# Kernel tuning notes

Measured on AMD Instinct MI355X. Metric: run time of the kernel, lower is better.

## Reference

```python
import jax, jax.numpy as jnp
import numpy as np


def _lstm_layer(x, w_ih, w_hh, b):
    """Single LSTM layer, PyTorch gate order (i, f, g, o).
    x: [B, T, Din]; w_ih: [4H, Din]; w_hh: [4H, H]; b: [4H] (= b_ih + b_hh).
    Returns hidden states [B, T, H]."""
    H = w_hh.shape[1]
    # Precompute input contribution for all timesteps at once (big GEMM).
    gates_x = jnp.einsum('btd,gd->btg', x, w_ih) + b  # [B, T, 4H]
    gates_t = jnp.swapaxes(gates_x, 0, 1)             # [T, B, 4H]
    B = x.shape[0]
    h0 = jnp.zeros((B, H), x.dtype)
    c0 = jnp.zeros((B, H), x.dtype)

    def step(carry, gx):
        h, c = carry
        g = gx + h @ w_hh.T                           # [B, 4H]
        i, f, gg, o = jnp.split(g, 4, axis=-1)
        i = jax.nn.sigmoid(i)
        f = jax.nn.sigmoid(f)
        gg = jnp.tanh(gg)
        o = jax.nn.sigmoid(o)
        c = f * c + i * gg
        h = o * jnp.tanh(c)
        return (h, c), h

    _, hs = jax.lax.scan(step, (h0, c0), gates_t)     # hs: [T, B, H]
    return jnp.swapaxes(hs, 0, 1)                     # [B, T, H]


def setup_inputs() -> dict:
    key = jax.random.key(0)
    ks = jax.random.split(key, 10)
    B, T, Din = 256, 256, 128
    Hemb = 512   # hidden_size (embed output)
    H = 512      # lstm_hidden_size
    L = 3        # nlayers
    Dout = 1     # output_size

    def unif(k, shape, bound):
        return jax.random.uniform(k, shape, jnp.float32, -bound, bound)

    s_emb = 1.0 / np.sqrt(Din)
    s_lstm = 1.0 / np.sqrt(H)
    s_dec = 1.0 / np.sqrt(H)

    return {
        'x': jax.random.normal(ks[0], (B, T, Din), jnp.float32),
        'embed_W': unif(ks[1], (Hemb, Din), s_emb),
        'embed_b': unif(ks[2], (Hemb,), s_emb),
        # stacked per-layer LSTM weights (hidden_size == lstm_hidden_size)
        'w_ih': unif(ks[3], (L, 4 * H, Hemb), s_lstm),
        'w_hh': unif(ks[4], (L, 4 * H, H), s_lstm),
        'b_ih': unif(ks[5], (L, 4 * H), s_lstm),
        'b_hh': unif(ks[6], (L, 4 * H), s_lstm),
        'dec_W': unif(ks[7], (Dout, H), s_dec),
        'dec_b': unif(ks[8], (Dout,), s_dec),
    }


def reference(x, embed_W, embed_b, w_ih, w_hh, b_ih, b_hh, dec_W, dec_b):
    # embed: Linear(input_size -> hidden_size)
    h = x @ embed_W.T + embed_b                       # [B, T, Hemb]
    # multi-layer LSTM (batch_first), zero initial state
    L = w_ih.shape[0]
    for l in range(L):
        h = _lstm_layer(h, w_ih[l], w_hh[l], b_ih[l] + b_hh[l])
    # decoder on last timestep, then flatten
    out = h[:, -1] @ dec_W.T + dec_b                  # [B, Dout]
    return out.reshape(-1)
```

## Files before the change

kernel.cpp:

```cpp
#include <hip/hip_runtime.h>
#include <hip/hip_fp16.h>
#include <cstdint>


#define TT   256
#define NBAT 256
#define DIN  128
#define HID  512
#define RD   16

typedef _Float16 half_t;
typedef __attribute__((ext_vector_type(8))) _Float16 half8;
typedef __attribute__((ext_vector_type(4))) _Float16 half4v;
typedef __attribute__((ext_vector_type(4))) float f32x4;

__device__ __forceinline__ float sigmoidf_(float x) {
    return 1.f / (1.f + __expf(-x));
}
__device__ __forceinline__ float tanhf_(float x) {
    float xc = fminf(fmaxf(x, -15.f), 15.f);
    float e = __expf(2.f * xc);
    return (e - 1.f) / (e + 1.f);
}

__device__ __forceinline__ half8 ld_cg16(const half_t* p) {
    union { unsigned long long u[2]; half8 v; } r;
    r.u[0] = __hip_atomic_load((const unsigned long long*)p,
                               __ATOMIC_RELAXED, __HIP_MEMORY_SCOPE_AGENT);
    r.u[1] = __hip_atomic_load((const unsigned long long*)p + 1,
                               __ATOMIC_RELAXED, __HIP_MEMORY_SCOPE_AGENT);
    return r.v;
}
__device__ __forceinline__ void st_cg2(half_t* p, float v) {
    half_t h = (half_t)v;
    unsigned short b = __builtin_bit_cast(unsigned short, h);
    __hip_atomic_store((unsigned short*)p, b,
                       __ATOMIC_RELAXED, __HIP_MEMORY_SCOPE_AGENT);
}

__device__ __forceinline__ void phase_out(float* Pl, const f32x4* accn,
                                          int wv, int lane) {
    #pragma unroll
    for (int n = 0; n < 4; ++n)
        #pragma unroll
        for (int q = 0; q < 4; ++q) {
            int prow = (wv << 4) + ((lane >> 4) << 2) + q;
            int cidx = (n << 4) + (lane & 15);
            Pl[prow * 64 + (cidx ^ ((((prow >> 2) ^ prow) & 1) << 4))] = accn[n][q];
        }
}
__device__ __forceinline__ float red_gates(const float* Pl, const float* b4,
                                           int rr, int jj, float& c) {
    float gs[4];
    #pragma unroll
    for (int gt = 0; gt < 4; ++gt) {
        float s = b4[gt];
        int cidx = (gt << 4) + jj;
        #pragma unroll
        for (int w2 = 0; w2 < 4; ++w2) {
            int r0 = (w2 << 4) + rr;
            s += Pl[r0 * 64 + (cidx ^ ((((r0 >> 2) ^ r0) & 1) << 4))];
        }
        gs[gt] = s;
    }
    float ig = sigmoidf_(gs[0]), fg = sigmoidf_(gs[1]);
    float gg = tanhf_(gs[2]), og = sigmoidf_(gs[3]);
    c = fg * c + ig * gg;
    return og * tanhf_(c);
}

__global__ __launch_bounds__(256) void k_w16(const float* __restrict__ wih,
                                             const float* __restrict__ whh,
                                             half_t* __restrict__ wbuf) {
    half8* wb = (half8*)wbuf;
    const int bid = blockIdx.x;
    const int l = bid >> 7;
    const int rem = bid & 127;
    const int hb = rem >> 2, q = rem & 3;
    const int tid = threadIdx.x;
    #pragma unroll
    for (int i = 0; i < 8; ++i) {
        int unit = tid + (i << 8);
        int kit = unit >> 8, n = (unit >> 6) & 3, lane = unit & 63;
        int grow = l * 2048 + n * 512 + hb * 16 + (lane & 15);
        int col = q * 256 + kit * 32 + ((lane >> 4) << 3);
        const float* src = (col < 512) ? (wih + (size_t)grow * HID + col)
                                       : (whh + (size_t)grow * HID + (col - 512));
        float4 u0 = *(const float4*)src;
        float4 u1 = *(const float4*)(src + 4);
        wb[((size_t)(l * 32 + hb) * 4 + q) * 2048 + unit] =
            (half8){(half_t)u0.x, (half_t)u0.y, (half_t)u0.z, (half_t)u0.w,
                    (half_t)u1.x, (half_t)u1.y, (half_t)u1.z, (half_t)u1.w};
    }
}

__global__ __launch_bounds__(256) void k_embed(const float* __restrict__ x,
                                               const float* __restrict__ W,
                                               const float* __restrict__ bias,
                                               half_t* __restrict__ out) {
    extern __shared__ char smem[];
    half_t* Xs = (half_t*)smem;
    half_t* Ws = (half_t*)(smem + 16384);
    const int tid = threadIdx.x;
    const int bk = blockIdx.x;
    const int t = bk >> 2, b0 = (bk & 3) << 6;

    #pragma unroll
    for (int it = 0; it < 8; ++it) {
        int idx = tid + (it << 8);
        int r = idx >> 5, k = (idx & 31) << 2;
        float4 v = *(const float4*)(x + ((size_t)(b0 + r) * TT + t) * DIN + k);
        half4v hv = {(half_t)v.x, (half_t)v.y, (half_t)v.z, (half_t)v.w};
        int byte = r * 256 + ((k * 2) ^ ((r & 7) << 4));
        *(half4v*)((char*)Xs + byte) = hv;
    }
    #pragma unroll 4
    for (int it = 0; it < 64; ++it) {
        int idx = tid + (it << 8);
        int r = idx >> 5, k = (idx & 31) << 2;
        float4 v = *(const float4*)(W + (size_t)r * DIN + k);
        half4v hv = {(half_t)v.x, (half_t)v.y, (half_t)v.z, (half_t)v.w};
        int byte = r * 256 + ((k * 2) ^ ((r & 7) << 4));
        *(half4v*)((char*)Ws + byte) = hv;
    }
    __syncthreads();

    const int lane = tid & 63, wv = tid >> 6;
    f32x4 acc[4][8];
    #pragma unroll
    for (int m = 0; m < 4; ++m)
        #pragma unroll
        for (int n = 0; n < 8; ++n) acc[m][n] = (f32x4){0.f, 0.f, 0.f, 0.f};

    #pragma unroll
    for (int kit = 0; kit < 4; ++kit) {
        int kk = (kit << 5) + ((lane >> 4) << 3);
        half8 a[4];
        #pragma unroll
        for (int m = 0; m < 4; ++m) {
            int r = (m << 4) + (lane & 15);
            int byte = r * 256 + ((kk * 2) ^ ((r & 7) << 4));
            a[m] = *(half8*)((char*)Xs + byte);
        }
        #pragma unroll
        for (int n = 0; n < 8; ++n) {
            int r = (wv << 7) + (n << 4) + (lane & 15);
            int byte = r * 256 + ((kk * 2) ^ ((r & 7) << 4));
            half8 b = *(half8*)((char*)Ws + byte);
            #pragma unroll
            for (int m = 0; m < 4; ++m)
                acc[m][n] = __builtin_amdgcn_mfma_f32_16x16x32_f16(a[m], b, acc[m][n], 0, 0, 0);
        }
    }
    __syncthreads();
    half_t* Os = (half_t*)smem;
    #pragma unroll
    for (int n = 0; n < 8; ++n) {
        int j = (wv << 7) + (n << 4) + (lane & 15);
        float bj = bias[j];
        #pragma unroll
        for (int m = 0; m < 4; ++m)
            #pragma unroll
            for (int r = 0; r < 4; ++r) {
                int mr = (m << 4) + ((lane >> 4) << 2) + r;
                Os[mr * 512 + j] = (half_t)(acc[m][n][r] + bj);
            }
    }
    __syncthreads();
    #pragma unroll
    for (int it = 0; it < 16; ++it) {
        int idx = tid + (it << 8);
        int r = idx >> 6, c = (idx & 63) << 3;
        half8 v = *(half8*)(Os + r * 512 + c);
        *(half8*)(out + ((size_t)t * NBAT + (b0 + r)) * HID + c) = v;
    }
}

__global__ __launch_bounds__(256, 1) void k_rec(const half_t* __restrict__ wbuf,
                                                const half_t* __restrict__ bufE,
                                                half_t* __restrict__ ring0,
                                                half_t* __restrict__ ring1,
                                                half_t* __restrict__ ring2,
                                                half_t* __restrict__ outbuf,
                                                const float* __restrict__ b_ih,
                                                const float* __restrict__ b_hh,
                                                int* __restrict__ flags) {
    extern __shared__ char smem[];
    half8* W2s = (half8*)smem;
    float* Pl = (float*)(smem + 131072);

    const half8* wb = (const half8*)wbuf;
    const int tid = threadIdx.x;
    const int lane = tid & 63, wv = tid >> 6;
    const int g = blockIdx.x & 7;
    const int hb = blockIdx.x >> 3;
    const int b0 = g << 5;
    const int j0 = hb << 4;
    const int rr = tid >> 4;
    const int jj = tid & 15;
    const bool low = (wv < 2);
    const int qw = wv ^ 2;
    const int koff = ((wv & 1) << 8) + ((lane >> 4) << 3);
    bool dead = false;

    half8 Bf0[8][4], Bf1[8][4];
    {
        const half8* w0 = wb + ((size_t)hb * 4 + wv) * 2048;
        const half8* w1 = wb + ((size_t)(32 + hb) * 4 + qw) * 2048;
        #pragma unroll
        for (int kit = 0; kit < 8; ++kit)
            #pragma unroll
            for (int n = 0; n < 4; ++n) {
                Bf0[kit][n] = w0[kit * 256 + n * 64 + lane];
                Bf1[kit][n] = w1[kit * 256 + n * 64 + lane];
            }
    }
    {
        const half8* w2 = wb + (size_t)(64 + hb) * 4 * 2048;
        #pragma unroll 4
        for (int it = 0; it < 32; ++it) {
            int idx = tid + (it << 8);
            W2s[idx] = w2[idx];
        }
    }
    float bias[3][4];
    #pragma unroll
    for (int l = 0; l < 3; ++l)
        #pragma unroll
        for (int gt = 0; gt < 4; ++gt)
            bias[l][gt] = b_ih[(size_t)l * 2048 + gt * HID + j0 + jj] +
                          b_hh[(size_t)l * 2048 + gt * HID + j0 + jj];
    float cA0 = 0.f, cA1 = 0.f, cB0 = 0.f, cB1 = 0.f, cC0 = 0.f, cC1 = 0.f;
    __syncthreads();

    const size_t RNG = (size_t)NBAT * HID;

    for (int r = 0; r < TT + 2; ++r) {
        const bool act0 = (r < TT);
        const bool act1 = (r >= 1 && r <= TT);
        const bool act2 = (r >= 2);

        if (tid < 96 && !dead) {
            int l = tid >> 5;
            int need = r - l; if (need > TT) need = TT;
            if (need > 0) {
                const int* fp = flags + l * 256 + (g << 5) + (tid & 31);
                int guard = 0;
                while (__hip_atomic_load(fp, __ATOMIC_RELAXED,
                                         __HIP_MEMORY_SCOPE_AGENT) < need) {
                    __builtin_amdgcn_s_sleep(1);
                    if (++guard > (1 << 17)) { dead = true; break; }
                }
            }
        }
        __syncthreads();

        half8 p0a[8], p0b[8];
        const size_t rowb = (size_t)(b0 + (lane & 15)) * HID + koff;
        if (low) {
            if (act0) {
                const half_t* ar = bufE + (size_t)r * RNG + rowb;
                #pragma unroll
                for (int kit = 0; kit < 8; ++kit) {
                    p0a[kit] = *(const half8*)(ar + (kit << 5));
                    p0b[kit] = *(const half8*)(ar + (size_t)16 * HID + (kit << 5));
                }
            }
        } else if (act1) {
            const half_t* ar = ring0 + (size_t)((r - 1) & (RD - 1)) * RNG + rowb;
            #pragma unroll
            for (int kit = 0; kit < 8; ++kit) {
                p0a[kit] = ld_cg16(ar + (kit << 5));
                p0b[kit] = ld_cg16(ar + (size_t)16 * HID + (kit << 5));
            }
        }

        f32x4 acc[2][4];

        #pragma unroll
        for (int m = 0; m < 2; ++m)
            #pragma unroll
            for (int n = 0; n < 4; ++n) acc[m][n] = (f32x4){0.f, 0.f, 0.f, 0.f};
        if (act0 && (low || r >= 1)) {
            #pragma unroll
            for (int kit = 0; kit < 8; ++kit)
                #pragma unroll
                for (int n = 0; n < 4; ++n) {
                    acc[0][n] = __builtin_amdgcn_mfma_f32_16x16x32_f16(p0a[kit], Bf0[kit][n], acc[0][n], 0, 0, 0);
                    acc[1][n] = __builtin_amdgcn_mfma_f32_16x16x32_f16(p0b[kit], Bf0[kit][n], acc[1][n], 0, 0, 0);
                }
        }
        half8 p1a[8], p1b[8];
        if (low && r >= 2) {
            const half_t* ar = ring1 + (size_t)((r - 2) & (RD - 1)) * RNG + rowb;
            #pragma unroll
            for (int kit = 0; kit < 8; ++kit) {
                p1a[kit] = ld_cg16(ar + (kit << 5));
                p1b[kit] = ld_cg16(ar + (size_t)16 * HID + (kit << 5));
            }
        }
        {
            half_t* dst = ring0 + (size_t)(r & (RD - 1)) * RNG;
            __syncthreads();
            phase_out(Pl, acc[0], wv, lane);
            __syncthreads();
            if (act0) st_cg2(dst + (size_t)(b0 + rr) * HID + j0 + jj,
                             red_gates(Pl, bias[0], rr, jj, cA0));
            __syncthreads();
            phase_out(Pl, acc[1], wv, lane);
            __syncthreads();
            if (act0) st_cg2(dst + (size_t)(b0 + 16 + rr) * HID + j0 + jj,
                             red_gates(Pl, bias[0], rr, jj, cA1));
        }

        #pragma unroll
        for (int m = 0; m < 2; ++m)
            #pragma unroll
            for (int n = 0; n < 4; ++n) acc[m][n] = (f32x4){0.f, 0.f, 0.f, 0.f};
        if (act1) {
            if (!low) {
                #pragma unroll
                for (int kit = 0; kit < 8; ++kit)
                    #pragma unroll
                    for (int n = 0; n < 4; ++n) {
                        acc[0][n] = __builtin_amdgcn_mfma_f32_16x16x32_f16(p0a[kit], Bf1[kit][n], acc[0][n], 0, 0, 0);
                        acc[1][n] = __builtin_amdgcn_mfma_f32_16x16x32_f16(p0b[kit], Bf1[kit][n], acc[1][n], 0, 0, 0);
                    }
            } else if (r >= 2) {
                #pragma unroll
                for (int kit = 0; kit < 8; ++kit)
                    #pragma unroll
                    for (int n = 0; n < 4; ++n) {
                        acc[0][n] = __builtin_amdgcn_mfma_f32_16x16x32_f16(p1a[kit], Bf1[kit][n], acc[0][n], 0, 0, 0);
                        acc[1][n] = __builtin_amdgcn_mfma_f32_16x16x32_f16(p1b[kit], Bf1[kit][n], acc[1][n], 0, 0, 0);
                    }
            }
        }
        if (!low && r >= 3) {
            const half_t* ar = ring2 + (size_t)((r - 3) & (RD - 1)) * RNG + rowb;
            #pragma unroll
            for (int kit = 0; kit < 8; ++kit) {
                p1a[kit] = ld_cg16(ar + (kit << 5));
                p1b[kit] = ld_cg16(ar + (size_t)16 * HID + (kit << 5));
            }
        }
        {
            half_t* dst = ring1 + (size_t)((r - 1) & (RD - 1)) * RNG;
            __syncthreads();
            phase_out(Pl, acc[0], wv, lane);
            __syncthreads();
            if (act1) st_cg2(dst + (size_t)(b0 + rr) * HID + j0 + jj,
                             red_gates(Pl, bias[1], rr, jj, cB0));
            __syncthreads();
            phase_out(Pl, acc[1], wv, lane);
            __syncthreads();
            if (act1) st_cg2(dst + (size_t)(b0 + 16 + rr) * HID + j0 + jj,
                             red_gates(Pl, bias[1], rr, jj, cB1));
        }

        #pragma unroll
        for (int m = 0; m < 2; ++m)
            #pragma unroll
            for (int n = 0; n < 4; ++n) acc[m][n] = (f32x4){0.f, 0.f, 0.f, 0.f};
        if (act2 && (low || r >= 3)) {
            const half8* w2l = W2s + ((size_t)wv << 11);
            #pragma unroll
            for (int kit = 0; kit < 8; ++kit) {
                half8 B0 = w2l[kit * 256 + 0 * 64 + lane];
                half8 B1 = w2l[kit * 256 + 1 * 64 + lane];
                half8 B2 = w2l[kit * 256 + 2 * 64 + lane];
                half8 B3 = w2l[kit * 256 + 3 * 64 + lane];
                acc[0][0] = __builtin_amdgcn_mfma_f32_16x16x32_f16(p1a[kit], B0, acc[0][0], 0, 0, 0);
                acc[1][0] = __builtin_amdgcn_mfma_f32_16x16x32_f16(p1b[kit], B0, acc[1][0], 0, 0, 0);
                acc[0][1] = __builtin_amdgcn_mfma_f32_16x16x32_f16(p1a[kit], B1, acc[0][1], 0, 0, 0);
                acc[1][1] = __builtin_amdgcn_mfma_f32_16x16x32_f16(p1b[kit], B1, acc[1][1], 0, 0, 0);
                acc[0][2] = __builtin_amdgcn_mfma_f32_16x16x32_f16(p1a[kit], B2, acc[0][2], 0, 0, 0);
                acc[1][2] = __builtin_amdgcn_mfma_f32_16x16x32_f16(p1b[kit], B2, acc[1][2], 0, 0, 0);
                acc[0][3] = __builtin_amdgcn_mfma_f32_16x16x32_f16(p1a[kit], B3, acc[0][3], 0, 0, 0);
                acc[1][3] = __builtin_amdgcn_mfma_f32_16x16x32_f16(p1b[kit], B3, acc[1][3], 0, 0, 0);
            }
        }
        {
            const int t2 = r - 2;
            half_t* dst = ring2 + (size_t)(t2 & (RD - 1)) * RNG;
            __syncthreads();
            phase_out(Pl, acc[0], wv, lane);
            __syncthreads();
            if (act2) {
                float h = red_gates(Pl, bias[2], rr, jj, cC0);
                st_cg2(dst + (size_t)(b0 + rr) * HID + j0 + jj, h);
                if (t2 == TT - 1)
                    st_cg2(outbuf + (size_t)(b0 + rr) * HID + j0 + jj, h);
            }
            __syncthreads();
            phase_out(Pl, acc[1], wv, lane);
            __syncthreads();
            if (act2) {
                float h = red_gates(Pl, bias[2], rr, jj, cC1);
                st_cg2(dst + (size_t)(b0 + 16 + rr) * HID + j0 + jj, h);
                if (t2 == TT - 1)
                    st_cg2(outbuf + (size_t)(b0 + 16 + rr) * HID + j0 + jj, h);
            }
        }

        asm volatile("s_waitcnt vmcnt(0)" ::: "memory");
        __builtin_amdgcn_sched_barrier(0);
        __syncthreads();
        if (tid == 0 && act0)
            __hip_atomic_store(flags + 0 * 256 + (g << 5) + hb, r + 1,
                               __ATOMIC_RELAXED, __HIP_MEMORY_SCOPE_AGENT);
        if (tid == 1 && act1)
            __hip_atomic_store(flags + 1 * 256 + (g << 5) + hb, r,
                               __ATOMIC_RELAXED, __HIP_MEMORY_SCOPE_AGENT);
        if (tid == 2 && act2)
            __hip_atomic_store(flags + 2 * 256 + (g << 5) + hb, r - 1,
                               __ATOMIC_RELAXED, __HIP_MEMORY_SCOPE_AGENT);
    }
}

__global__ __launch_bounds__(256) void k_dec(const half_t* __restrict__ act,
                                             const float* __restrict__ dW,
                                             const float* __restrict__ db,
                                             float* __restrict__ out) {
    int tid = threadIdx.x;
    int bl = tid >> 3, part = tid & 7;
    int b = (blockIdx.x << 5) + bl;
    const half_t* row = act + (size_t)b * HID + (part << 6);
    float s = 0.f;
    #pragma unroll
    for (int i = 0; i < 8; ++i) {
        half8 v = ld_cg16(row + (i << 3));
        const float* wp = dW + (part << 6) + (i << 3);
        #pragma unroll
        for (int u = 0; u < 8; ++u) s += (float)v[u] * wp[u];
    }
    #pragma unroll
    for (int off = 1; off < 8; off <<= 1) s += __shfl_xor(s, off, 64);
    if (part == 0) out[b] = s + db[0];
}

extern "C" void kernel_launch(void* const* d_in, const int* in_sizes, int n_in,
                              void* d_out, int out_size, void* d_ws, size_t ws_size,
                              hipStream_t stream) {
    const float* x = (const float*)d_in[0];
    const float* eW = (const float*)d_in[1];
    const float* eb = (const float*)d_in[2];
    const float* wih = (const float*)d_in[3];
    const float* whh = (const float*)d_in[4];
    const float* bih = (const float*)d_in[5];
    const float* bhh = (const float*)d_in[6];
    const float* dW = (const float*)d_in[7];
    const float* db = (const float*)d_in[8];
    float* out = (float*)d_out;

    const size_t MB = 1u << 20;
    const size_t BUFE_OFF = 0;
    const size_t RING0_OFF = 64 * MB;
    const size_t RING1_OFF = 68 * MB;
    const size_t RING2_OFF = 72 * MB;
    const size_t OUT_OFF = 76 * MB;
    const size_t WBUF_OFF = 80 * MB;
    const size_t FLAG_OFF = 96 * MB;
    if (ws_size < 96 * MB + 65536) return;

    char* ws = (char*)d_ws;
    half_t* bufE = (half_t*)(ws + BUFE_OFF);
    half_t* ring0 = (half_t*)(ws + RING0_OFF);
    half_t* ring1 = (half_t*)(ws + RING1_OFF);
    half_t* ring2 = (half_t*)(ws + RING2_OFF);
    half_t* outbuf = (half_t*)(ws + OUT_OFF);
    half_t* wbuf = (half_t*)(ws + WBUF_OFF);
    int* flags = (int*)(ws + FLAG_OFF);

    hipMemsetAsync(flags, 0, 1024 * sizeof(int), stream);

    (void)hipFuncSetAttribute((const void*)k_embed,
                              hipFuncAttributeMaxDynamicSharedMemorySize, 147456);
    (void)hipFuncSetAttribute((const void*)k_rec,
                              hipFuncAttributeMaxDynamicSharedMemorySize, 147456);

    k_w16<<<384, 256, 0, stream>>>(wih, whh, wbuf);
    k_embed<<<1024, 256, 147456, stream>>>(x, eW, eb, bufE);

    void* args[] = { (void*)&wbuf, (void*)&bufE, (void*)&ring0, (void*)&ring1,
                     (void*)&ring2, (void*)&outbuf, (void*)&bih, (void*)&bhh,
                     (void*)&flags };
    hipError_t ce = hipLaunchCooperativeKernel((const void*)k_rec, dim3(256), dim3(256),
                                               args, 147456, stream);
    if (ce != hipSuccess) {
        k_rec<<<256, 256, 147456, stream>>>(wbuf, bufE, ring0, ring1, ring2,
                                            outbuf, bih, bhh, flags);
    }

    k_dec<<<8, 256, 0, stream>>>(outbuf, dW, db, out);
}
```

Before: 2.970 ms.

## Split recurrent LSTM kernel K-reduction across eight waves per block

Doubles the recurrent kernel's block size to 512 threads so each wave covers a quarter of the hidden dimension, halving per-wave MFMA chains and register-held weight fragments. Partial gate sums from 8 waves are reduced through a larger LDS staging area, with only the first 256 threads applying the gate nonlinearities. Some redundant barriers are removed. The intent is to shorten the per-timestep critical path and improve latency hiding, at the cost of more LDS traffic in the reduction and tighter register limits from the new launch bounds.

Measured after the change: 4.181 ms. +40.8%, slower.

```diff
diff --git a/kernel.cpp b/kernel.cpp
--- a/kernel.cpp
+++ b/kernel.cpp
@@ -39,12 +39,12 @@
 }
 
 __device__ __forceinline__ void phase_out(float* Pl, const f32x4* accn,
-                                          int wv, int lane) {
+                                          int w, int lane) {
     #pragma unroll
     for (int n = 0; n < 4; ++n)
         #pragma unroll
         for (int q = 0; q < 4; ++q) {
-            int prow = (wv << 4) + ((lane >> 4) << 2) + q;
+            int prow = (w << 4) + ((lane >> 4) << 2) + q;
             int cidx = (n << 4) + (lane & 15);
             Pl[prow * 64 + (cidx ^ ((((prow >> 2) ^ prow) & 1) << 4))] = accn[n][q];
         }
@@ -57,8 +57,8 @@
         float s = b4[gt];
         int cidx = (gt << 4) + jj;
         #pragma unroll
-        for (int w2 = 0; w2 < 4; ++w2) {
-            int r0 = (w2 << 4) + rr;
+        for (int w8 = 0; w8 < 8; ++w8) {
+            int r0 = (w8 << 4) + rr;
             s += Pl[r0 * 64 + (cidx ^ ((((r0 >> 2) ^ r0) & 1) << 4))];
         }
         gs[gt] = s;
@@ -176,7 +176,7 @@
     }
 }
 
-__global__ __launch_bounds__(256, 1) void k_rec(const half_t* __restrict__ wbuf,
+__global__ __launch_bounds__(512, 2) void k_rec(const half_t* __restrict__ wbuf,
                                                 const half_t* __restrict__ bufE,
                                                 half_t* __restrict__ ring0,
                                                 half_t* __restrict__ ring1,
@@ -191,24 +191,25 @@
 
     const half8* wb = (const half8*)wbuf;
     const int tid = threadIdx.x;
-    const int lane = tid & 63, wv = tid >> 6;
+    const int lane = tid & 63, w = tid >> 6;
     const int g = blockIdx.x & 7;
     const int hb = blockIdx.x >> 3;
     const int b0 = g << 5;
     const int j0 = hb << 4;
     const int rr = tid >> 4;
     const int jj = tid & 15;
-    const bool low = (wv < 2);
-    const int qw = wv ^ 2;
-    const int koff = ((wv & 1) << 8) + ((lane >> 4) << 3);
+    const bool low = (w < 4);
+    const int wsub = w & 3;
+    const int koff = (wsub << 7) + ((lane >> 4) << 3);
+    const int wq1 = w ^ 4;
     bool dead = false;
 
-    half8 Bf0[8][4], Bf1[8][4];
+    half8 Bf0[4][4], Bf1[4][4];
     {
-        const half8* w0 = wb + ((size_t)hb * 4 + wv) * 2048;
-        const half8* w1 = wb + ((size_t)(32 + hb) * 4 + qw) * 2048;
-        #pragma unroll
-        for (int kit = 0; kit < 8; ++kit)
+        const half8* w0 = wb + ((size_t)hb * 4 + (w >> 1)) * 2048 + ((w & 1) << 10);
+        const half8* w1 = wb + ((size_t)(32 + hb) * 4 + (wq1 >> 1)) * 2048 + ((wq1 & 1) << 10);
+        #pragma unroll
+        for (int kit = 0; kit < 4; ++kit)
             #pragma unroll
             for (int n = 0; n < 4; ++n) {
                 Bf0[kit][n] = w0[kit * 256 + n * 64 + lane];
@@ -218,8 +219,8 @@
     {
         const half8* w2 = wb + (size_t)(64 + hb) * 4 * 2048;
         #pragma unroll 4
-        for (int it = 0; it < 32; ++it) {
-            int idx = tid + (it << 8);
+        for (int it = 0; it < 16; ++it) {
+            int idx = tid + (it << 9);
             W2s[idx] = w2[idx];
         }
     }
@@ -234,6 +235,7 @@
     __syncthreads();
 
     const size_t RNG = (size_t)NBAT * HID;
+    const bool red = (tid < 256);
 
     for (int r = 0; r < TT + 2; ++r) {
         const bool act0 = (r < TT);
@@ -255,13 +257,13 @@
         }
         __syncthreads();
 
-        half8 p0a[8], p0b[8];
+        half8 p0a[4], p0b[4];
         const size_t rowb = (size_t)(b0 + (lane & 15)) * HID + koff;
         if (low) {
             if (act0) {
                 const half_t* ar = bufE + (size_t)r * RNG + rowb;
                 #pragma unroll
-                for (int kit = 0; kit < 8; ++kit) {
+                for (int kit = 0; kit < 4; ++kit) {
                     p0a[kit] = *(const half8*)(ar + (kit << 5));
                     p0b[kit] = *(const half8*)(ar + (size_t)16 * HID + (kit << 5));
                 }
@@ -269,7 +271,7 @@
         } else if (act1) {
             const half_t* ar = ring0 + (size_t)((r - 1) & (RD - 1)) * RNG + rowb;
             #pragma unroll
-            for (int kit = 0; kit < 8; ++kit) {
+            for (int kit = 0; kit < 4; ++kit) {
                 p0a[kit] = ld_cg16(ar + (kit << 5));
                 p0b[kit] = ld_cg16(ar + (size_t)16 * HID + (kit << 5));
             }
@@ -283,35 +285,35 @@
             for (int n = 0; n < 4; ++n) acc[m][n] = (f32x4){0.f, 0.f, 0.f, 0.f};
         if (act0 && (low || r >= 1)) {
             #pragma unroll
-            for (int kit = 0; kit < 8; ++kit)
+            for (int kit = 0; kit < 4; ++kit)
                 #pragma unroll
                 for (int n = 0; n < 4; ++n) {
                     acc[0][n] = __builtin_amdgcn_mfma_f32_16x16x32_f16(p0a[kit], Bf0[kit][n], acc[0][n], 0, 0, 0);
                     acc[1][n] = __builtin_amdgcn_mfma_f32_16x16x32_f16(p0b[kit], Bf0[kit][n], acc[1][n], 0, 0, 0);
                 }
         }
-        half8 p1a[8], p1b[8];
+        half8 p1a[4], p1b[4];
         if (low && r >= 2) {
             const half_t* ar = ring1 + (size_t)((r - 2) & (RD - 1)) * RNG + rowb;
             #pragma unroll
-            for (int kit = 0; kit < 8; ++kit) {
+            for (int kit = 0; kit < 4; ++kit) {
                 p1a[kit] = ld_cg16(ar + (kit << 5));
                 p1b[kit] = ld_cg16(ar + (size_t)16 * HID + (kit << 5));
             }
         }
         {
             half_t* dst = ring0 + (size_t)(r & (RD - 1)) * RNG;
-            __syncthreads();
-            phase_out(Pl, acc[0], wv, lane);
-            __syncthreads();
-            if (act0) st_cg2(dst + (size_t)(b0 + rr) * HID + j0 + jj,
-                             red_gates(Pl, bias[0], rr, jj, cA0));
-            __syncthreads();
-            phase_out(Pl, acc[1], wv, lane);
-            __syncthreads();
-            if (act0) st_cg2(dst + (size_t)(b0 + 16 + rr) * HID + j0 + jj,
-                             red_gates(Pl, bias[0], rr, jj, cA1));
-        }
+            phase_out(Pl, acc[0], w, lane);
+            __syncthreads();
+            if (red && act0) st_cg2(dst + (size_t)(b0 + rr) * HID + j0 + jj,
+                                    red_gates(Pl, bias[0], rr, jj, cA0));
+            __syncthreads();
+            phase_out(Pl, acc[1], w, lane);
+            __syncthreads();
+            if (red && act0) st_cg2(dst + (size_t)(b0 + 16 + rr) * HID + j0 + jj,
+                                    red_gates(Pl, bias[0], rr, jj, cA1));
+        }
+        __syncthreads();
 
         #pragma unroll
         for (int m = 0; m < 2; ++m)
@@ -320,7 +322,7 @@
         if (act1) {
             if (!low) {
                 #pragma unroll
-                for (int kit = 0; kit < 8; ++kit)
+                for (int kit = 0; kit < 4; ++kit)
                     #pragma unroll
                     for (int n = 0; n < 4; ++n) {
                         acc[0][n] = __builtin_amdgcn_mfma_f32_16x16x32_f16(p0a[kit], Bf1[kit][n], acc[0][n], 0, 0, 0);
@@ -328,7 +330,7 @@
                     }
             } else if (r >= 2) {
                 #pragma unroll
-                for (int kit = 0; kit < 8; ++kit)
+                for (int kit = 0; kit < 4; ++kit)
                     #pragma unroll
                     for (int n = 0; n < 4; ++n) {
                         acc[0][n] = __builtin_amdgcn_mfma_f32_16x16x32_f16(p1a[kit], Bf1[kit][n], acc[0][n], 0, 0, 0);
@@ -339,33 +341,33 @@
         if (!low && r >= 3) {
             const half_t* ar = ring2 + (size_t)((r - 3) & (RD - 1)) * RNG + rowb;
             #pragma unroll
-            for (int kit = 0; kit < 8; ++kit) {
+            for (int kit = 0; kit < 4; ++kit) {
                 p1a[kit] = ld_cg16(ar + (kit << 5));
                 p1b[kit] = ld_cg16(ar + (size_t)16 * HID + (kit << 5));
             }
         }
         {
             half_t* dst = ring1 + (size_t)((r - 1) & (RD - 1)) * RNG;
-            __syncthreads();
-            phase_out(Pl, acc[0], wv, lane);
-            __syncthreads();
-            if (act1) st_cg2(dst + (size_t)(b0 + rr) * HID + j0 + jj,
-                             red_gates(Pl, bias[1], rr, jj, cB0));
-            __syncthreads();
-            phase_out(Pl, acc[1], wv, lane);
-            __syncthreads();
-            if (act1) st_cg2(dst + (size_t)(b0 + 16 + rr) * HID + j0 + jj,
-                             red_gates(Pl, bias[1], rr, jj, cB1));
-        }
+            phase_out(Pl, acc[0], w, lane);
+            __syncthreads();
+            if (red && act1) st_cg2(dst + (size_t)(b0 + rr) * HID + j0 + jj,
+                                    red_gates(Pl, bias[1], rr, jj, cB0));
+            __syncthreads();
+            phase_out(Pl, acc[1], w, lane);
+            __syncthreads();
+            if (red && act1) st_cg2(dst + (size_t)(b0 + 16 + rr) * HID + j0 + jj,
+                                    red_gates(Pl, bias[1], rr, jj, cB1));
+        }
+        __syncthreads();
 
         #pragma unroll
         for (int m = 0; m < 2; ++m)
             #pragma unroll
             for (int n = 0; n < 4; ++n) acc[m][n] = (f32x4){0.f, 0.f, 0.f, 0.f};
         if (act2 && (low || r >= 3)) {
-            const half8* w2l = W2s + ((size_t)wv << 11);
-            #pragma unroll
-            for (int kit = 0; kit < 8; ++kit) {
+            const half8* w2l = W2s + (((size_t)(w >> 1) << 11) + ((w & 1) << 10));
+            #pragma unroll
+            for (int kit = 0; kit < 4; ++kit) {
                 half8 B0 = w2l[kit * 256 + 0 * 64 + lane];
                 half8 B1 = w2l[kit * 256 + 1 * 64 + lane];
                 half8 B2 = w2l[kit * 256 + 2 * 64 + lane];
@@ -383,19 +385,18 @@
         {
             const int t2 = r - 2;
             half_t* dst = ring2 + (size_t)(t2 & (RD - 1)) * RNG;
-            __syncthreads();
-            phase_out(Pl, acc[0], wv, lane);
-            __syncthreads();
-            if (act2) {
+            phase_out(Pl, acc[0], w, lane);
+            __syncthreads();
+            if (red && act2) {
                 float h = red_gates(Pl, bias[2], rr, jj, cC0);
                 st_cg2(dst + (size_t)(b0 + rr) * HID + j0 + jj, h);
                 if (t2 == TT - 1)
                     st_cg2(outbuf + (size_t)(b0 + rr) * HID + j0 + jj, h);
             }
             __syncthreads();
-            phase_out(Pl, acc[1], wv, lane);
-            __syncthreads();
-            if (act2) {
+            phase_out(Pl, acc[1], w, lane);
+            __syncthreads();
+            if (red && act2) {
                 float h = red_gates(Pl, bias[2], rr, jj, cC1);
                 st_cg2(dst + (size_t)(b0 + 16 + rr) * HID + j0 + jj, h);
                 if (t2 == TT - 1)
@@ -477,7 +478,7 @@
     (void)hipFuncSetAttribute((const void*)k_embed,
                               hipFuncAttributeMaxDynamicSharedMemorySize, 147456);
     (void)hipFuncSetAttribute((const void*)k_rec,
-                              hipFuncAttributeMaxDynamicSharedMemorySize, 147456);
+                              hipFuncAttributeMaxDynamicSharedMemorySize, 163840);
 
     k_w16<<<384, 256, 0, stream>>>(wih, whh, wbuf);
     k_embed<<<1024, 256, 147456, stream>>>(x, eW, eb, bufE);
@@ -485,10 +486,10 @@
     void* args[] = { (void*)&wbuf, (void*)&bufE, (void*)&ring0, (void*)&ring1,
                      (void*)&ring2, (void*)&outbuf, (void*)&bih, (void*)&bhh,
                      (void*)&flags };
-    hipError_t ce = hipLaunchCooperativeKernel((const void*)k_rec, dim3(256), dim3(256),
-                                               args, 147456, stream);
+    hipError_t ce = hipLaunchCooperativeKernel((const void*)k_rec, dim3(256), dim3(512),
+                                               args, 163840, stream);
     if (ce != hipSuccess) {
-        k_rec<<<256, 256, 147456, stream>>>(wbuf, bufE, ring0, ring1, ring2,
+        k_rec<<<256, 512, 163840, stream>>>(wbuf, bufE, ring0, ring1, ring2,
                                             outbuf, bih, bhh, flags);
     }
 
```

## Use full-length ring buffers with cached loads and merge gate reduction phases

Applied to the files above, without the earlier changes.

When enough workspace is available, each layer's ring buffer is enlarged to hold all timesteps. Slots are then never reused, so consumers can read them with ordinary cached loads instead of agent-scope atomic loads. Both 16-row accumulator halves are now written to a larger LDS staging area at once, which cuts the per-layer barriers from four to two and raises dynamic shared memory to 160 KiB. The risk is stale cached data if a cache line holding a not-yet-written slot is fetched before the producer stores it, plus much higher workspace use.

Result: no change. 2.944 ms (-0.9%).

```diff
diff --git a/kernel.cpp b/kernel.cpp
--- a/kernel.cpp
+++ b/kernel.cpp
@@ -7,7 +7,6 @@
 #define NBAT 256
 #define DIN  128
 #define HID  512
-#define RD   16
 
 typedef _Float16 half_t;
 typedef __attribute__((ext_vector_type(8))) _Float16 half8;
@@ -38,19 +37,21 @@
                        __ATOMIC_RELAXED, __HIP_MEMORY_SCOPE_AGENT);
 }
 
-__device__ __forceinline__ void phase_out(float* Pl, const f32x4* accn,
-                                          int wv, int lane) {
-    #pragma unroll
-    for (int n = 0; n < 4; ++n)
-        #pragma unroll
-        for (int q = 0; q < 4; ++q) {
-            int prow = (wv << 4) + ((lane >> 4) << 2) + q;
-            int cidx = (n << 4) + (lane & 15);
-            Pl[prow * 64 + (cidx ^ ((((prow >> 2) ^ prow) & 1) << 4))] = accn[n][q];
-        }
-}
-__device__ __forceinline__ float red_gates(const float* Pl, const float* b4,
-                                           int rr, int jj, float& c) {
+__device__ __forceinline__ void phase_out2(float* Pl, const f32x4 acc[2][4],
+                                           int wv, int lane) {
+    #pragma unroll
+    for (int m = 0; m < 2; ++m)
+        #pragma unroll
+        for (int n = 0; n < 4; ++n)
+            #pragma unroll
+            for (int q = 0; q < 4; ++q) {
+                int prow = (wv << 5) + (m << 4) + ((lane >> 4) << 2) + q;
+                int cidx = (n << 4) + (lane & 15);
+                Pl[prow * 64 + (cidx ^ ((((prow >> 2) ^ prow) & 1) << 4))] = acc[m][n][q];
+            }
+}
+__device__ __forceinline__ float red_gatesS(const float* Pl, const float* b4,
+                                            int brow, int jj, float& c) {
     float gs[4];
     #pragma unroll
     for (int gt = 0; gt < 4; ++gt) {
@@ -58,7 +59,7 @@
         int cidx = (gt << 4) + jj;
         #pragma unroll
         for (int w2 = 0; w2 < 4; ++w2) {
-            int r0 = (w2 << 4) + rr;
+            int r0 = (w2 << 5) + brow;
             s += Pl[r0 * 64 + (cidx ^ ((((r0 >> 2) ^ r0) & 1) << 4))];
         }
         gs[gt] = s;
@@ -184,7 +185,8 @@
                                                 half_t* __restrict__ outbuf,
                                                 const float* __restrict__ b_ih,
                                                 const float* __restrict__ b_hh,
-                                                int* __restrict__ flags) {
+                                                int* __restrict__ flags,
+                                                int rdmask, int cached) {
     extern __shared__ char smem[];
     half8* W2s = (half8*)smem;
     float* Pl = (float*)(smem + 131072);
@@ -267,11 +269,19 @@
                 }
             }
         } else if (act1) {
-            const half_t* ar = ring0 + (size_t)((r - 1) & (RD - 1)) * RNG + rowb;
-            #pragma unroll
-            for (int kit = 0; kit < 8; ++kit) {
-                p0a[kit] = ld_cg16(ar + (kit << 5));
-                p0b[kit] = ld_cg16(ar + (size_t)16 * HID + (kit << 5));
+            const half_t* ar = ring0 + (size_t)((r - 1) & rdmask) * RNG + rowb;
+            if (cached) {
+                #pragma unroll
+                for (int kit = 0; kit < 8; ++kit) {
+                    p0a[kit] = *(const half8*)(ar + (kit << 5));
+                    p0b[kit] = *(const half8*)(ar + (size_t)16 * HID + (kit << 5));
+                }
+            } else {
+                #pragma unroll
+                for (int kit = 0; kit < 8; ++kit) {
+                    p0a[kit] = ld_cg16(ar + (kit << 5));
+                    p0b[kit] = ld_cg16(ar + (size_t)16 * HID + (kit << 5));
+                }
             }
         }
 
@@ -292,25 +302,32 @@
         }
         half8 p1a[8], p1b[8];
         if (low && r >= 2) {
-            const half_t* ar = ring1 + (size_t)((r - 2) & (RD - 1)) * RNG + rowb;
-            #pragma unroll
-            for (int kit = 0; kit < 8; ++kit) {
-                p1a[kit] = ld_cg16(ar + (kit << 5));
-                p1b[kit] = ld_cg16(ar + (size_t)16 * HID + (kit << 5));
+            const half_t* ar = ring1 + (size_t)((r - 2) & rdmask) * RNG + rowb;
+            if (cached) {
+                #pragma unroll
+                for (int kit = 0; kit < 8; ++kit) {
+                    p1a[kit] = *(const half8*)(ar + (kit << 5));
+                    p1b[kit] = *(const half8*)(ar + (size_t)16 * HID + (kit << 5));
+                }
+            } else {
+                #pragma unroll
+                for (int kit = 0; kit < 8; ++kit) {
+                    p1a[kit] = ld_cg16(ar + (kit << 5));
+                    p1b[kit] = ld_cg16(ar + (size_t)16 * HID + (kit << 5));
+                }
             }
         }
         {
-            half_t* dst = ring0 + (size_t)(r & (RD - 1)) * RNG;
+            half_t* dst = ring0 + (size_t)(r & rdmask) * RNG;
+            phase_out2(Pl, acc, wv, lane);
             __syncthreads();
-            phase_out(Pl, acc[0], wv, lane);
+            if (act0) {
+                st_cg2(dst + (size_t)(b0 + rr) * HID + j0 + jj,
+                       red_gatesS(Pl, bias[0], rr, jj, cA0));
+                st_cg2(dst + (size_t)(b0 + 16 + rr) * HID + j0 + jj,
+                       red_gatesS(Pl, bias[0], 16 + rr, jj, cA1));
+            }
             __syncthreads();
-            if (act0) st_cg2(dst + (size_t)(b0 + rr) * HID + j0 + jj,
-                             red_gates(Pl, bias[0], rr, jj, cA0));
-            __syncthreads();
-            phase_out(Pl, acc[1], wv, lane);
-            __syncthreads();
-            if (act0) st_cg2(dst + (size_t)(b0 + 16 + rr) * HID + j0 + jj,
-                             red_gates(Pl, bias[0], rr, jj, cA1));
         }
 
         #pragma unroll
@@ -337,25 +354,32 @@
             }
         }
         if (!low && r >= 3) {
-            const half_t* ar = ring2 + (size_t)((r - 3) & (RD - 1)) * RNG + rowb;
-            #pragma unroll
-            for (int kit = 0; kit < 8; ++kit) {
-                p1a[kit] = ld_cg16(ar + (kit << 5));
-                p1b[kit] = ld_cg16(ar + (size_t)16 * HID + (kit << 5));
+            const half_t* ar = ring2 + (size_t)((r - 3) & rdmask) * RNG + rowb;
+            if (cached) {
+                #pragma unroll
+                for (int kit = 0; kit < 8; ++kit) {
+                    p1a[kit] = *(const half8*)(ar + (kit << 5));
+                    p1b[kit] = *(const half8*)(ar + (size_t)16 * HID + (kit << 5));
+                }
+            } else {
+                #pragma unroll
+                for (int kit = 0; kit < 8; ++kit) {
+                    p1a[kit] = ld_cg16(ar + (kit << 5));
+                    p1b[kit] = ld_cg16(ar + (size_t)16 * HID + (kit << 5));
+                }
             }
         }
         {
-            half_t* dst = ring1 + (size_t)((r - 1) & (RD - 1)) * RNG;
+            half_t* dst = ring1 + (size_t)((r - 1) & rdmask) * RNG;
+            phase_out2(Pl, acc, wv, lane);
             __syncthreads();
-            phase_out(Pl, acc[0], wv, lane);
+            if (act1) {
+                st_cg2(dst + (size_t)(b0 + rr) * HID + j0 + jj,
+                       red_gatesS(Pl, bias[1], rr, jj, cB0));
+                st_cg2(dst + (size_t)(b0 + 16 + rr) * HID + j0 + jj,
+                       red_gatesS(Pl, bias[1], 16 + rr, jj, cB1));
+            }
             __syncthreads();
-            if (act1) st_cg2(dst + (size_t)(b0 + rr) * HID + j0 + jj,
-                             red_gates(Pl, bias[1], rr, jj, cB0));
-            __syncthreads();
-            phase_out(Pl, acc[1], wv, lane);
-            __syncthreads();
-            if (act1) st_cg2(dst + (size_t)(b0 + 16 + rr) * HID + j0 + jj,
-                             red_gates(Pl, bias[1], rr, jj, cB1));
         }
 
         #pragma unroll
@@ -382,24 +406,18 @@
         }
         {
             const int t2 = r - 2;
-            half_t* dst = ring2 + (size_t)(t2 & (RD - 1)) * RNG;
-            __syncthreads();
-            phase_out(Pl, acc[0], wv, lane);
+            half_t* dst = ring2 + (size_t)(t2 & rdmask) * RNG;
+            phase_out2(Pl, acc, wv, lane);
             __syncthreads();
             if (act2) {
-                float h = red_gates(Pl, bias[2], rr, jj, cC0);
-                st_cg2(dst + (size_t)(b0 + rr) * HID + j0 + jj, h);
-                if (t2 == TT - 1)
-                    st_cg2(outbuf + (size_t)(b0 + rr) * HID + j0 + jj, h);
-            }
-            __syncthreads();
-            phase_out(Pl, acc[1], wv, lane);
-            __syncthreads();
-            if (act2) {
-                float h = red_gates(Pl, bias[2], rr, jj, cC1);
-                st_cg2(dst + (size_t)(b0 + 16 + rr) * HID + j0 + jj, h);
-                if (t2 == TT - 1)
-                    st_cg2(outbuf + (size_t)(b0 + 16 + rr) * HID + j0 + jj, h);
+                float h0v = red_gatesS(Pl, bias[2], rr, jj, cC0);
+                float h1v = red_gatesS(Pl, bias[2], 16 + rr, jj, cC1);
+                st_cg2(dst + (size_t)(b0 + rr) * HID + j0 + jj, h0v);
+                st_cg2(dst + (size_t)(b0 + 16 + rr) * HID + j0 + jj, h1v);
+                if (t2 == TT - 1) {
+                    st_cg2(outbuf + (size_t)(b0 + rr) * HID + j0 + jj, h0v);
+                    st_cg2(outbuf + (size_t)(b0 + 16 + rr) * HID + j0 + jj, h1v);
+                }
             }
         }
 
@@ -454,42 +472,52 @@
     float* out = (float*)d_out;
 
     const size_t MB = 1u << 20;
-    const size_t BUFE_OFF = 0;
-    const size_t RING0_OFF = 64 * MB;
-    const size_t RING1_OFF = 68 * MB;
-    const size_t RING2_OFF = 72 * MB;
-    const size_t OUT_OFF = 76 * MB;
-    const size_t WBUF_OFF = 80 * MB;
-    const size_t FLAG_OFF = 96 * MB;
+    const size_t RINGFULL = 64 * MB;
+    const size_t FULL_NEED = 270 * MB + 65536;
+    const bool full = (ws_size >= FULL_NEED);
     if (ws_size < 96 * MB + 65536) return;
 
     char* ws = (char*)d_ws;
-    half_t* bufE = (half_t*)(ws + BUFE_OFF);
-    half_t* ring0 = (half_t*)(ws + RING0_OFF);
-    half_t* ring1 = (half_t*)(ws + RING1_OFF);
-    half_t* ring2 = (half_t*)(ws + RING2_OFF);
-    half_t* outbuf = (half_t*)(ws + OUT_OFF);
-    half_t* wbuf = (half_t*)(ws + WBUF_OFF);
-    int* flags = (int*)(ws + FLAG_OFF);
+    half_t* bufE = (half_t*)ws;
+    half_t *ring0, *ring1, *ring2, *outbuf, *wbuf;
+    int* flags;
+    int rdmask, cached;
+    if (full) {
+        ring0 = (half_t*)(ws + 64 * MB);
+        ring1 = (half_t*)(ws + 128 * MB);
+        ring2 = (half_t*)(ws + 192 * MB);
+        outbuf = (half_t*)(ws + 256 * MB);
+        wbuf = (half_t*)(ws + 257 * MB);
+        flags = (int*)(ws + 270 * MB);
+        rdmask = 255; cached = 1;
+    } else {
+        ring0 = (half_t*)(ws + 64 * MB);
+        ring1 = (half_t*)(ws + 68 * MB);
+        ring2 = (half_t*)(ws + 72 * MB);
+        outbuf = (half_t*)(ws + 76 * MB);
+        wbuf = (half_t*)(ws + 80 * MB);
+        flags = (int*)(ws + 96 * MB);
+        rdmask = 15; cached = 0;
+    }
 
     hipMemsetAsync(flags, 0, 1024 * sizeof(int), stream);
 
     (void)hipFuncSetAttribute((const void*)k_embed,
                               hipFuncAttributeMaxDynamicSharedMemorySize, 147456);
     (void)hipFuncSetAttribute((const void*)k_rec,
-                              hipFuncAttributeMaxDynamicSharedMemorySize, 147456);
+                              hipFuncAttributeMaxDynamicSharedMemorySize, 163840);
 
     k_w16<<<384, 256, 0, stream>>>(wih, whh, wbuf);
     k_embed<<<1024, 256, 147456, stream>>>(x, eW, eb, bufE);
 
     void* args[] = { (void*)&wbuf, (void*)&bufE, (void*)&ring0, (void*)&ring1,
                      (void*)&ring2, (void*)&outbuf, (void*)&bih, (void*)&bhh,
-                     (void*)&flags };
+                     (void*)&flags, (void*)&rdmask, (void*)&cached };
     hipError_t ce = hipLaunchCooperativeKernel((const void*)k_rec, dim3(256), dim3(256),
-                                               args, 147456, stream);
+                                               args, 163840, stream);
     if (ce != hipSuccess) {
-        k_rec<<<256, 256, 147456, stream>>>(wbuf, bufE, ring0, ring1, ring2,
-                                            outbuf, bih, bhh, flags);
+        k_rec<<<256, 256, 163840, stream>>>(wbuf, bufE, ring0, ring1, ring2,
+                                            outbuf, bih, bhh, flags, rdmask, cached);
     }
 
     k_dec<<<8, 256, 0, stream>>>(outbuf, dW, db, out);
```
